# Kernel optimization log

Measured on AMD Instinct MI355X. Metric: run time of the kernel, lower is better.

## Reference

```python
import jax, jax.numpy as jnp
import numpy as np

B, N, D, K = 2, 8192, 512, 16


def setup_inputs() -> dict:
    key = jax.random.key(0)
    k1, k2, k3, k4 = jax.random.split(key, 4)
    x = jax.random.normal(k1, (B, N, D), dtype=jnp.float32)
    xyz = jax.random.normal(k2, (B, N, 3), dtype=jnp.float32)
    # nn.Linear(d_model, 3*d_model): weight [3D, D], bias [3D]
    W_qkv = jax.random.normal(k3, (3 * D, D), dtype=jnp.float32) * 0.02
    b_qkv = jnp.zeros((3 * D,), dtype=jnp.float32)
    # nn.Linear(d_model, d_model)
    W_fc = jax.random.normal(k4, (D, D), dtype=jnp.float32) * 0.02
    b_fc = jnp.zeros((D,), dtype=jnp.float32)
    return {"x": x, "xyz": xyz, "W_qkv": W_qkv, "b_qkv": b_qkv, "W_fc": W_fc, "b_fc": b_fc}


def _knn_idx(xyz):
    # squared-distance KNN (same ordering as cdist): |a|^2 + |b|^2 - 2 a.b
    sq = jnp.sum(xyz * xyz, axis=-1)                      # [B, N]
    d2 = sq[:, :, None] + sq[:, None, :] - 2.0 * jnp.einsum('bnc,bmc->bnm', xyz, xyz)
    return jax.lax.top_k(-d2, K)[1]                       # [B, N, K] smallest distances


def reference(x, xyz, W_qkv, b_qkv, W_fc, b_fc):
    knn_idx = _knn_idx(xyz)                               # no-grad in original
    qkv = jnp.einsum('bnd,ed->bne', x, W_qkv) + b_qkv     # [B, N, 3D]
    qkv = qkv.reshape(B, N, 3, D)
    q, k, v = qkv[:, :, 0], qkv[:, :, 1], qkv[:, :, 2]    # [B, N, D]
    gather = jax.vmap(lambda arr, idx: arr[idx])          # per-batch neighbor gather
    k_neigh = gather(k, knn_idx)                          # [B, N, K, D]
    v_neigh = gather(v, knn_idx)                          # [B, N, K, D]
    # faithful to einsum('bnd,bnsk->bns', q, k_neigh): sums d and feature dims independently
    attn = (q.sum(-1)[:, :, None] * k_neigh.sum(-1)) / jnp.sqrt(jnp.float32(D))  # [B, N, K]
    attn = jax.nn.softmax(attn, axis=2)[..., None]        # [B, N, K, 1]
    x_out = (attn * v_neigh).sum(axis=2)                  # [B, N, D]
    return jnp.einsum('bnd,ed->bne', x_out, W_fc) + b_fc + x
```

## Files before the change

kernel.cpp:

```cpp
#include <hip/hip_runtime.h>

typedef _Float16 half_t;
typedef _Float16 half8 __attribute__((ext_vector_type(8)));
typedef _Float16 half4v __attribute__((ext_vector_type(4)));
typedef float f32x4 __attribute__((ext_vector_type(4)));
typedef float f32x2 __attribute__((ext_vector_type(2)));

#define NB 2
#define NN 8192
#define ND 512
#define NKNN 16
#define BN (NB*NN)

#define OFF_XH   0ull
#define OFF_VH   (OFF_XH  + (size_t)BN*ND*2)
#define OFF_XOH  (OFF_VH  + (size_t)BN*ND*2)
#define OFF_WVH  (OFF_XOH + (size_t)BN*ND*2)
#define OFF_WFCH (OFF_WVH + (size_t)ND*ND*2)
#define OFF_XW   (OFF_WFCH+ (size_t)ND*ND*2)
#define OFF_XW2  (OFF_XW  + (size_t)BN*16)
#define OFF_IDX  (OFF_XW2 + (size_t)BN*16)
#define OFF_WQC  (OFF_IDX + (size_t)BN*NKNN*4)
#define OFF_WKC  (OFF_WQC + 2048)
#define OFF_QKB  (OFF_WKC + 2048)
#define OFF_QS   (OFF_QKB + 256)
#define OFF_KS   (OFF_QS  + (size_t)BN*4)

__device__ __forceinline__ void gload16(const void* g, void* l) {
  __builtin_amdgcn_global_load_lds((const __attribute__((address_space(1))) void*)g,
                                   (__attribute__((address_space(3))) void*)l, 16, 0, 0);
}

__global__ __launch_bounds__(256) void ksetup(const float* __restrict__ wqkv,
                                              const float* __restrict__ bqkv,
                                              const float* __restrict__ wfc,
                                              const float* __restrict__ xyz,
                                              float* __restrict__ wq, float* __restrict__ wk,
                                              float* __restrict__ qkb,
                                              half_t* __restrict__ wvh, half_t* __restrict__ wfch,
                                              float4* __restrict__ xw, float4* __restrict__ xw2) {
  const int blk = blockIdx.x;
  const int t = threadIdx.x;
  if (blk < 16) {
    int h = blk >> 3, g = blk & 7;
    int dl = t & 63, s = t >> 6;
    const float* Wb = wqkv + (size_t)h * 512 * 512;
    int d = g * 64 + dl;
    float acc = 0.f;
    for (int e = s * 128; e < s * 128 + 128; ++e) acc += Wb[(size_t)e * 512 + d];
    __shared__ float red[4][64];
    red[s][dl] = acc;
    __syncthreads();
    if (s == 0) (h ? wk : wq)[d] = red[0][dl] + red[1][dl] + red[2][dl] + red[3][dl];
  } else if (blk == 16) {
    __shared__ float r0[256], r1[256];
    r0[t] = bqkv[t] + bqkv[t + 256];
    r1[t] = bqkv[512 + t] + bqkv[768 + t];
    __syncthreads();
    for (int s = 128; s; s >>= 1) {
      if (t < s) { r0[t] += r0[t + s]; r1[t] += r1[t + s]; }
      __syncthreads();
    }
    if (t == 0) { qkb[0] = r0[0]; qkb[1] = r1[0]; }
  } else if (blk < 273) {
    int i = (blk - 17) * 256 + t;
    float4 a = ((const float4*)(wqkv + 1024 * 512))[i];
    half4v ha; ha[0]=(half_t)a.x; ha[1]=(half_t)a.y; ha[2]=(half_t)a.z; ha[3]=(half_t)a.w;
    *(half4v*)(wvh + (size_t)i * 4) = ha;
    float4 c = ((const float4*)wfc)[i];
    half4v hc; hc[0]=(half_t)c.x; hc[1]=(half_t)c.y; hc[2]=(half_t)c.z; hc[3]=(half_t)c.w;
    *(half4v*)(wfch + (size_t)i * 4) = hc;
  } else {
    int p = (blk - 273) * 256 + t;
    int b = p >> 12;
    int pl = p & 4095;
    int i0 = b * NN + pl * 2;
    const float* s = xyz + (size_t)i0 * 3;
    float x0 = s[0], y0 = s[1], z0 = s[2];
    float x1 = s[3], y1 = s[4], z1 = s[5];
    float sq0 = __fadd_rn(__fadd_rn(__fmul_rn(x0, x0), __fmul_rn(y0, y0)), __fmul_rn(z0, z0));
    float sq1 = __fadd_rn(__fadd_rn(__fmul_rn(x1, x1), __fmul_rn(y1, y1)), __fmul_rn(z1, z1));
    xw[i0]     = make_float4(x0, y0, z0, sq0);
    xw[i0 + 1] = make_float4(x1, y1, z1, sq1);
    xw2[(size_t)b * NN + pl]        = make_float4(x0, x1, y0, y1);
    xw2[(size_t)b * NN + NN/2 + pl] = make_float4(z0, z1, sq0, sq1);
  }
}

__global__ __launch_bounds__(256) void kxh(const float* __restrict__ x,
                                           const float* __restrict__ wq,
                                           const float* __restrict__ wk,
                                           const float* __restrict__ qkb,
                                           half_t* __restrict__ xh,
                                           float* __restrict__ qs,
                                           float* __restrict__ ks) {
  int wid = blockIdx.x * 4 + (threadIdx.x >> 6);
  int l = threadIdx.x & 63;
  size_t base = (size_t)wid * ND + l * 8;
  float4 a0 = *(const float4*)(x + base);
  float4 a1 = *(const float4*)(x + base + 4);
  half8 h;
  h[0]=(half_t)a0.x; h[1]=(half_t)a0.y; h[2]=(half_t)a0.z; h[3]=(half_t)a0.w;
  h[4]=(half_t)a1.x; h[5]=(half_t)a1.y; h[6]=(half_t)a1.z; h[7]=(half_t)a1.w;
  *(half8*)(xh + base) = h;
  float4 q0 = ((const float4*)(wq + l * 8))[0], q1 = ((const float4*)(wq + l * 8))[1];
  float4 k0 = ((const float4*)(wk + l * 8))[0], k1 = ((const float4*)(wk + l * 8))[1];
  float dq = a0.x*q0.x + a0.y*q0.y + a0.z*q0.z + a0.w*q0.w
           + a1.x*q1.x + a1.y*q1.y + a1.z*q1.z + a1.w*q1.w;
  float dk = a0.x*k0.x + a0.y*k0.y + a0.z*k0.z + a0.w*k0.w
           + a1.x*k1.x + a1.y*k1.y + a1.z*k1.z + a1.w*k1.w;
  #pragma unroll
  for (int o = 32; o; o >>= 1) { dq += __shfl_xor(dq, o); dk += __shfl_xor(dk, o); }
  if (l == 0) { qs[wid] = dq + qkb[0]; ks[wid] = dk + qkb[1]; }
}

#define QPW 4
#define KTILE 512
__global__ __launch_bounds__(256, 4) void kknn(const float4* __restrict__ xw,
                                               const float4* __restrict__ xw2,
                                               int* __restrict__ idxo) {
  __shared__ __align__(16) float4 ldsA[2][KTILE];
  __shared__ __align__(16) float4 ldsB[2][KTILE];
  __shared__ float qdl[16 * 64];
  __shared__ int   qil[16 * 64];
  const int tid = threadIdx.x;
  const int l = tid & 63;
  const int w = tid >> 6;
  const int b = blockIdx.x >> 9;
  const int qbase = (blockIdx.x & 511) * (4 * QPW) + w * QPW;
  const float4* xb  = xw  + (size_t)b * NN;
  const float4* xa2 = xw2 + (size_t)b * NN;
  const float4* xb2 = xa2 + NN / 2;

#define STAGE(t, bi) do {                                                        \
    int ts_ = (t) * KTILE;                                                       \
    gload16(xa2 + ts_ +       w * 64 + l, (void*)&ldsA[bi][      w * 64]);       \
    gload16(xa2 + ts_ + 256 + w * 64 + l, (void*)&ldsA[bi][256 + w * 64]);       \
    gload16(xb2 + ts_ +       w * 64 + l, (void*)&ldsB[bi][      w * 64]);       \
    gload16(xb2 + ts_ + 256 + w * 64 + l, (void*)&ldsB[bi][256 + w * 64]);       \
  } while (0)

  f32x2 qxx[QPW], qyy[QPW], qzz[QPW], qww[QPW];
  #pragma unroll
  for (int qi = 0; qi < QPW; ++qi) {
    float4 qp = xb[qbase + qi];
    qxx[qi] = (f32x2){qp.x, qp.x};
    qyy[qi] = (f32x2){qp.y, qp.y};
    qzz[qi] = (f32x2){qp.z, qp.z};
    qww[qi] = (f32x2){qp.w, qp.w};
  }
  const f32x2 m2 = (f32x2){-2.0f, -2.0f};

  #pragma unroll
  for (int qi = 0; qi < QPW; ++qi) {
    qdl[(w * 4 + qi) * 64 + l] = __builtin_inff();
    qil[(w * 4 + qi) * 64 + l] = 0x7fffffff;
  }

  f32x2 mind[QPW];
  #pragma unroll
  for (int qi = 0; qi < QPW; ++qi) mind[qi] = (f32x2){__builtin_inff(), __builtin_inff()};

  STAGE(0, 0);
  __syncthreads();
  for (int t = 0; t < 8; ++t) {
    if (t < 7) STAGE(t + 1, (t + 1) & 1);
    #pragma unroll
    for (int it = 0; it < 8; ++it) {
      int p = it * 64 + l;
      float4 A  = ldsA[t & 1][p];
      float4 Bv = ldsB[t & 1][p];
      f32x2 cx = (f32x2){A.x, A.y};
      f32x2 cy = (f32x2){A.z, A.w};
      f32x2 cz = (f32x2){Bv.x, Bv.y};
      f32x2 cw = (f32x2){Bv.z, Bv.w};
      #pragma unroll
      for (int qi = 0; qi < QPW; ++qi) {
        f32x2 dot = __builtin_elementwise_fma(qzz[qi], cz,
                      __builtin_elementwise_fma(qyy[qi], cy, qxx[qi] * cx));
        f32x2 s2 = qww[qi] + cw;
        f32x2 d2 = __builtin_elementwise_fma(m2, dot, s2);
        mind[qi] = __builtin_elementwise_min(mind[qi], d2);
      }
    }
    __syncthreads();
  }

  float wst[QPW];
  #pragma unroll
  for (int qi = 0; qi < QPW; ++qi) {
    float d = fminf(mind[qi][0], mind[qi][1]);
    #pragma unroll
    for (int k = 2; k <= 64; k <<= 1) {
      #pragma unroll
      for (int j = k >> 1; j > 0; j >>= 1) {
        float od = __shfl_xor(d, j);
        bool up = ((l & k) == 0);
        bool lower_lane = ((l & j) == 0);
        bool oless = od < d;
        bool take = (up == lower_lane) ? oless : !oless;
        if (take) d = od;
      }
    }
    wst[qi] = __shfl(d, 15);
  }

  int qcnt[QPW];
  #pragma unroll
  for (int qi = 0; qi < QPW; ++qi) qcnt[qi] = 0;
  const unsigned long long below = (l == 63) ? ~0ull >> 1 : (1ull << l) - 1;

  __syncthreads();
  STAGE(0, 0);
  __syncthreads();
  for (int t = 0; t < 8; ++t) {
    if (t < 7) STAGE(t + 1, (t + 1) & 1);
    #pragma unroll 2
    for (int it = 0; it < 8; ++it) {
      int p = it * 64 + l;
      float4 A  = ldsA[t & 1][p];
      float4 Bv = ldsB[t & 1][p];
      f32x2 cx = (f32x2){A.x, A.y};
      f32x2 cy = (f32x2){A.z, A.w};
      f32x2 cz = (f32x2){Bv.x, Bv.y};
      f32x2 cw = (f32x2){Bv.z, Bv.w};
      int ci0 = (t * KTILE + p) * 2;
      #pragma unroll
      for (int qi = 0; qi < QPW; ++qi) {
        f32x2 dot = __builtin_elementwise_fma(qzz[qi], cz,
                      __builtin_elementwise_fma(qyy[qi], cy, qxx[qi] * cx));
        f32x2 s2 = qww[qi] + cw;
        f32x2 d2 = __builtin_elementwise_fma(m2, dot, s2);
        bool ok0 = d2[0] <= wst[qi];
        bool ok1 = d2[1] <= wst[qi];
        unsigned long long m0 = __ballot(ok0);
        if (m0) {
          int slot = qcnt[qi] + __popcll(m0 & below);
          if (ok0 && slot < 64) {
            qdl[(w * 4 + qi) * 64 + slot] = d2[0];
            qil[(w * 4 + qi) * 64 + slot] = ci0;
          }
          qcnt[qi] += __popcll(m0);
        }
        unsigned long long m1 = __ballot(ok1);
        if (m1) {
          int slot = qcnt[qi] + __popcll(m1 & below);
          if (ok1 && slot < 64) {
            qdl[(w * 4 + qi) * 64 + slot] = d2[1];
            qil[(w * 4 + qi) * 64 + slot] = ci0 + 1;
          }
          qcnt[qi] += __popcll(m1);
        }
      }
    }
    __syncthreads();
  }

  #pragma unroll
  for (int qi = 0; qi < QPW; ++qi) {
    float d = qdl[(w * 4 + qi) * 64 + l];
    int  ii = qil[(w * 4 + qi) * 64 + l];
    #pragma unroll
    for (int k = 2; k <= 64; k <<= 1) {
      #pragma unroll
      for (int j = k >> 1; j > 0; j >>= 1) {
        float od = __shfl_xor(d, j);
        int   oi = __shfl_xor(ii, j);
        bool up = ((l & k) == 0);
        bool lower_lane = ((l & j) == 0);
        bool oless = (od < d) || (od == d && oi < ii);
        bool take = (up == lower_lane) ? oless : !oless;
        if (take) { d = od; ii = oi; }
      }
    }
    if (l < 16) idxo[((size_t)b * NN + qbase + qi) * NKNN + l] = ii;
  }
#undef STAGE
}

template <int EPI>
__global__ __launch_bounds__(256) void kgemm(const half_t* __restrict__ A,
                                             const half_t* __restrict__ Bw,
                                             const float* __restrict__ bias,
                                             const float* __restrict__ resid,
                                             void* __restrict__ Cout) {
  __shared__ __align__(16) half_t As[128 * 64];
  __shared__ __align__(16) half_t Bs[128 * 64];
  const int tid = threadIdx.x;
  const int l = tid & 63;
  const int w = tid >> 6;
  const int wm = w >> 1, wn = w & 1;
  const int mt = blockIdx.x >> 2;
  const int nt = blockIdx.x & 3;
  const int lr = l & 15, lg = l >> 4;

  f32x4 acc[4][4];
  #pragma unroll
  for (int i = 0; i < 4; ++i)
    #pragma unroll
    for (int j = 0; j < 4; ++j) acc[i][j] = (f32x4){0.f, 0.f, 0.f, 0.f};

  for (int kt = 0; kt < 8; ++kt) {
    #pragma unroll
    for (int i = 0; i < 4; ++i) {
      int id = i * 256 + tid;
      int rr = id >> 3, cc = id & 7;
      gload16(A + (size_t)(mt * 128 + rr) * ND + kt * 64 + cc * 8,
              (void*)(As + (size_t)(i * 256 + w * 64) * 8));
      gload16(Bw + (size_t)(nt * 128 + rr) * ND + kt * 64 + cc * 8,
              (void*)(Bs + (size_t)(i * 256 + w * 64) * 8));
    }
    __syncthreads();
    #pragma unroll
    for (int kk = 0; kk < 2; ++kk) {
      half8 af[4], bf[4];
      #pragma unroll
      for (int mi = 0; mi < 4; ++mi)
        af[mi] = *(const half8*)(As + (wm * 64 + mi * 16 + lr) * 64 + kk * 32 + lg * 8);
      #pragma unroll
      for (int ni = 0; ni < 4; ++ni)
        bf[ni] = *(const half8*)(Bs + (wn * 64 + ni * 16 + lr) * 64 + kk * 32 + lg * 8);
      #pragma unroll
      for (int mi = 0; mi < 4; ++mi)
        #pragma unroll
        for (int ni = 0; ni < 4; ++ni)
          acc[mi][ni] = __builtin_amdgcn_mfma_f32_16x16x32_f16(af[mi], bf[ni], acc[mi][ni], 0, 0, 0);
    }
    __syncthreads();
  }

  #pragma unroll
  for (int mi = 0; mi < 4; ++mi) {
    #pragma unroll
    for (int ni = 0; ni < 4; ++ni) {
      int col = nt * 128 + wn * 64 + ni * 16 + lr;
      #pragma unroll
      for (int r4 = 0; r4 < 4; ++r4) {
        size_t row = (size_t)mt * 128 + wm * 64 + mi * 16 + lg * 4 + r4;
        float v = acc[mi][ni][r4] + bias[col];
        if (EPI == 0) ((half_t*)Cout)[row * ND + col] = (half_t)v;
        else          ((float*)Cout)[row * ND + col] = v + resid[row * ND + col];
      }
    }
  }
}

__global__ __launch_bounds__(256) void kattn(const int* __restrict__ idx,
                                             const float* __restrict__ qs,
                                             const float* __restrict__ ks,
                                             const half_t* __restrict__ vh,
                                             half_t* __restrict__ xoh) {
  int wid = blockIdx.x * 4 + (threadIdx.x >> 6);
  int l = threadIdx.x & 63;
  int b = wid >> 13;
  int j = l & 15;
  int nb = idx[(size_t)wid * NKNN + j];
  float ksv = ks[(size_t)b * NN + nb];
  float logit = __fdiv_rn(__fmul_rn(qs[wid], ksv), 22.627416997969522f);
  float mx = logit;
  #pragma unroll
  for (int o = 8; o; o >>= 1) mx = fmaxf(mx, __shfl_xor(mx, o, 16));
  float e = expf(logit - mx);
  float s = e;
  #pragma unroll
  for (int o = 8; o; o >>= 1) s += __shfl_xor(s, o, 16);
  float p = e / s;

  float acc[8] = {0.f, 0.f, 0.f, 0.f, 0.f, 0.f, 0.f, 0.f};
  #pragma unroll
  for (int t16 = 0; t16 < 16; ++t16) {
    float wj = __shfl(p, t16, 16);
    int ij = __shfl(nb, t16, 16);
    const half8 vv = *(const half8*)(vh + ((size_t)b * NN + ij) * ND + l * 8);
    #pragma unroll
    for (int u = 0; u < 8; ++u) acc[u] += wj * (float)vv[u];
  }
  half8 ho;
  #pragma unroll
  for (int u = 0; u < 8; ++u) ho[u] = (half_t)acc[u];
  *(half8*)(xoh + (size_t)wid * ND + l * 8) = ho;
}

extern "C" void kernel_launch(void* const* d_in, const int* in_sizes, int n_in,
                              void* d_out, int out_size, void* d_ws, size_t ws_size,
                              hipStream_t stream) {
  const float* x    = (const float*)d_in[0];
  const float* xyz  = (const float*)d_in[1];
  const float* wqkv = (const float*)d_in[2];
  const float* bqkv = (const float*)d_in[3];
  const float* wfc  = (const float*)d_in[4];
  const float* bfc  = (const float*)d_in[5];
  char* ws = (char*)d_ws;
  half_t* xh   = (half_t*)(ws + OFF_XH);
  half_t* vh   = (half_t*)(ws + OFF_VH);
  half_t* xoh  = (half_t*)(ws + OFF_XOH);
  half_t* wvh  = (half_t*)(ws + OFF_WVH);
  half_t* wfch = (half_t*)(ws + OFF_WFCH);
  float4* xw   = (float4*)(ws + OFF_XW);
  float4* xw2  = (float4*)(ws + OFF_XW2);
  int*    idx  = (int*)(ws + OFF_IDX);
  float*  wqc  = (float*)(ws + OFF_WQC);
  float*  wkc  = (float*)(ws + OFF_WKC);
  float*  qkb  = (float*)(ws + OFF_QKB);
  float*  qs   = (float*)(ws + OFF_QS);
  float*  ks   = (float*)(ws + OFF_KS);

  ksetup<<<dim3(305), dim3(256), 0, stream>>>(wqkv, bqkv, wfc, xyz,
                                              wqc, wkc, qkb, wvh, wfch, xw, xw2);
  kxh   <<<dim3(4096),dim3(256), 0, stream>>>(x, wqc, wkc, qkb, xh, qs, ks);
  kknn  <<<dim3(1024),dim3(256), 0, stream>>>(xw, xw2, idx);
  kgemm<0><<<dim3(512),dim3(256), 0, stream>>>(xh, wvh, bqkv + 1024, (const float*)nullptr, (void*)vh);
  kattn <<<dim3(4096),dim3(256), 0, stream>>>(idx, qs, ks, vh, xoh);
  kgemm<1><<<dim3(512),dim3(256), 0, stream>>>(xoh, wfch, bfc, x, d_out);
}
```

Baseline: 145.3 us.

## Fold output projection into value projection to drop the final GEMM

Result: no change. 142.9 us (median of 2 runs) (-1.7%).

```diff
diff --git a/kernel.cpp b/kernel.cpp
--- a/kernel.cpp
+++ b/kernel.cpp
@@ -25,6 +25,8 @@
 #define OFF_QKB  (OFF_WKC + 2048)
 #define OFF_QS   (OFF_QKB + 256)
 #define OFF_KS   (OFF_QS  + (size_t)BN*4)
+#define OFF_WCB  OFF_XOH
+#define OFF_BCB  (OFF_XOH + (size_t)ND*ND*2)
 
 __device__ __forceinline__ void gload16(const void* g, void* l) {
   __builtin_amdgcn_global_load_lds((const __attribute__((address_space(1))) void*)g,
@@ -37,8 +39,9 @@
                                               const float* __restrict__ xyz,
                                               float* __restrict__ wq, float* __restrict__ wk,
                                               float* __restrict__ qkb,
-                                              half_t* __restrict__ wvh, half_t* __restrict__ wfch,
-                                              float4* __restrict__ xw, float4* __restrict__ xw2) {
+                                              half_t* __restrict__ wvth, half_t* __restrict__ wfch,
+                                              float4* __restrict__ xw, float4* __restrict__ xw2,
+                                              float* __restrict__ bcomb) {
   const int blk = blockIdx.x;
   const int t = threadIdx.x;
   if (blk < 16) {
@@ -64,13 +67,10 @@
     if (t == 0) { qkb[0] = r0[0]; qkb[1] = r1[0]; }
   } else if (blk < 273) {
     int i = (blk - 17) * 256 + t;
-    float4 a = ((const float4*)(wqkv + 1024 * 512))[i];
-    half4v ha; ha[0]=(half_t)a.x; ha[1]=(half_t)a.y; ha[2]=(half_t)a.z; ha[3]=(half_t)a.w;
-    *(half4v*)(wvh + (size_t)i * 4) = ha;
     float4 c = ((const float4*)wfc)[i];
     half4v hc; hc[0]=(half_t)c.x; hc[1]=(half_t)c.y; hc[2]=(half_t)c.z; hc[3]=(half_t)c.w;
     *(half4v*)(wfch + (size_t)i * 4) = hc;
-  } else {
+  } else if (blk < 305) {
     int p = (blk - 273) * 256 + t;
     int b = p >> 12;
     int pl = p & 4095;
@@ -84,6 +84,31 @@
     xw[i0 + 1] = make_float4(x1, y1, z1, sq1);
     xw2[(size_t)b * NN + pl]        = make_float4(x0, x1, y0, y1);
     xw2[(size_t)b * NN + NN/2 + pl] = make_float4(z0, z1, sq0, sq1);
+  } else if (blk < 369) {
+    int tile = blk - 305, tr = tile >> 3, tc = tile & 7;
+    __shared__ float tbuf[64][65];
+    int rr = t >> 6, cc = t & 63;
+    #pragma unroll 4
+    for (int p = 0; p < 16; ++p)
+      tbuf[p * 4 + rr][cc] = wqkv[(size_t)(1024 + tc * 64 + p * 4 + rr) * 512 + tr * 64 + cc];
+    __syncthreads();
+    #pragma unroll 4
+    for (int p = 0; p < 16; ++p)
+      wvth[(size_t)(tr * 64 + p * 4 + rr) * 512 + tc * 64 + cc] = (half_t)tbuf[cc][p * 4 + rr];
+  } else {
+    int base = (blk - 369) * 8;
+    int wv_ = t >> 6, l_ = t & 63;
+    #pragma unroll
+    for (int rr = 0; rr < 2; ++rr) {
+      int e = base + wv_ * 2 + rr;
+      float acc = 0.f;
+      #pragma unroll
+      for (int it = 0; it < 8; ++it)
+        acc += wfc[(size_t)e * 512 + it * 64 + l_] * bqkv[1024 + it * 64 + l_];
+      #pragma unroll
+      for (int o = 32; o; o >>= 1) acc += __shfl_xor(acc, o);
+      if (l_ == 0) bcomb[e] = acc;
+    }
   }
 }
 
@@ -208,7 +233,7 @@
   int qcnt[QPW];
   #pragma unroll
   for (int qi = 0; qi < QPW; ++qi) qcnt[qi] = 0;
-  const unsigned long long below = (l == 63) ? ~0ull >> 1 : (1ull << l) - 1;
+  const unsigned long long below = (1ull << l) - 1;
 
   __syncthreads();
   STAGE(0, 0);
@@ -282,7 +307,6 @@
 __global__ __launch_bounds__(256) void kgemm(const half_t* __restrict__ A,
                                              const half_t* __restrict__ Bw,
                                              const float* __restrict__ bias,
-                                             const float* __restrict__ resid,
                                              void* __restrict__ Cout) {
   __shared__ __align__(16) half_t As[128 * 64];
   __shared__ __align__(16) half_t Bs[128 * 64];
@@ -337,9 +361,8 @@
       #pragma unroll
       for (int r4 = 0; r4 < 4; ++r4) {
         size_t row = (size_t)mt * 128 + wm * 64 + mi * 16 + lg * 4 + r4;
-        float v = acc[mi][ni][r4] + bias[col];
-        if (EPI == 0) ((half_t*)Cout)[row * ND + col] = (half_t)v;
-        else          ((float*)Cout)[row * ND + col] = v + resid[row * ND + col];
+        if (EPI == 0) ((half_t*)Cout)[row * ND + col] = (half_t)(acc[mi][ni][r4] + bias[col]);
+        else          ((half_t*)Cout)[row * ND + col] = (half_t)acc[mi][ni][r4];
       }
     }
   }
@@ -348,8 +371,10 @@
 __global__ __launch_bounds__(256) void kattn(const int* __restrict__ idx,
                                              const float* __restrict__ qs,
                                              const float* __restrict__ ks,
-                                             const half_t* __restrict__ vh,
-                                             half_t* __restrict__ xoh) {
+                                             const half_t* __restrict__ vfh,
+                                             const float* __restrict__ bfc,
+                                             const float* __restrict__ x,
+                                             float* __restrict__ out) {
   int wid = blockIdx.x * 4 + (threadIdx.x >> 6);
   int l = threadIdx.x & 63;
   int b = wid >> 13;
@@ -371,14 +396,21 @@
   for (int t16 = 0; t16 < 16; ++t16) {
     float wj = __shfl(p, t16, 16);
     int ij = __shfl(nb, t16, 16);
-    const half8 vv = *(const half8*)(vh + ((size_t)b * NN + ij) * ND + l * 8);
+    const half8 vv = *(const half8*)(vfh + ((size_t)b * NN + ij) * ND + l * 8);
     #pragma unroll
     for (int u = 0; u < 8; ++u) acc[u] += wj * (float)vv[u];
   }
-  half8 ho;
-  #pragma unroll
-  for (int u = 0; u < 8; ++u) ho[u] = (half_t)acc[u];
-  *(half8*)(xoh + (size_t)wid * ND + l * 8) = ho;
+  size_t base = (size_t)wid * ND + l * 8;
+  float4 xa0 = *(const float4*)(x + base);
+  float4 xa1 = *(const float4*)(x + base + 4);
+  float4 bf0 = *(const float4*)(bfc + l * 8);
+  float4 bf1 = *(const float4*)(bfc + l * 8 + 4);
+  float4 o0 = make_float4(acc[0] + bf0.x + xa0.x, acc[1] + bf0.y + xa0.y,
+                          acc[2] + bf0.z + xa0.z, acc[3] + bf0.w + xa0.w);
+  float4 o1 = make_float4(acc[4] + bf1.x + xa1.x, acc[5] + bf1.y + xa1.y,
+                          acc[6] + bf1.z + xa1.z, acc[7] + bf1.w + xa1.w);
+  *(float4*)(out + base) = o0;
+  *(float4*)(out + base + 4) = o1;
 }
 
 extern "C" void kernel_launch(void* const* d_in, const int* in_sizes, int n_in,
@@ -391,25 +423,26 @@
   const float* wfc  = (const float*)d_in[4];
   const float* bfc  = (const float*)d_in[5];
   char* ws = (char*)d_ws;
-  half_t* xh   = (half_t*)(ws + OFF_XH);
-  half_t* vh   = (half_t*)(ws + OFF_VH);
-  half_t* xoh  = (half_t*)(ws + OFF_XOH);
-  half_t* wvh  = (half_t*)(ws + OFF_WVH);
-  half_t* wfch = (half_t*)(ws + OFF_WFCH);
-  float4* xw   = (float4*)(ws + OFF_XW);
-  float4* xw2  = (float4*)(ws + OFF_XW2);
-  int*    idx  = (int*)(ws + OFF_IDX);
-  float*  wqc  = (float*)(ws + OFF_WQC);
-  float*  wkc  = (float*)(ws + OFF_WKC);
-  float*  qkb  = (float*)(ws + OFF_QKB);
-  float*  qs   = (float*)(ws + OFF_QS);
-  float*  ks   = (float*)(ws + OFF_KS);
-
-  ksetup<<<dim3(305), dim3(256), 0, stream>>>(wqkv, bqkv, wfc, xyz,
-                                              wqc, wkc, qkb, wvh, wfch, xw, xw2);
-  kxh   <<<dim3(4096),dim3(256), 0, stream>>>(x, wqc, wkc, qkb, xh, qs, ks);
-  kknn  <<<dim3(1024),dim3(256), 0, stream>>>(xw, xw2, idx);
-  kgemm<0><<<dim3(512),dim3(256), 0, stream>>>(xh, wvh, bqkv + 1024, (const float*)nullptr, (void*)vh);
-  kattn <<<dim3(4096),dim3(256), 0, stream>>>(idx, qs, ks, vh, xoh);
-  kgemm<1><<<dim3(512),dim3(256), 0, stream>>>(xoh, wfch, bfc, x, d_out);
-}
+  half_t* xh    = (half_t*)(ws + OFF_XH);
+  half_t* vfh   = (half_t*)(ws + OFF_VH);
+  half_t* wvth  = (half_t*)(ws + OFF_WVH);
+  half_t* wfch  = (half_t*)(ws + OFF_WFCH);
+  half_t* wcomb = (half_t*)(ws + OFF_WCB);
+  float*  bcomb = (float*)(ws + OFF_BCB);
+  float4* xw    = (float4*)(ws + OFF_XW);
+  float4* xw2   = (float4*)(ws + OFF_XW2);
+  int*    idx   = (int*)(ws + OFF_IDX);
+  float*  wqc   = (float*)(ws + OFF_WQC);
+  float*  wkc   = (float*)(ws + OFF_WKC);
+  float*  qkb   = (float*)(ws + OFF_QKB);
+  float*  qs    = (float*)(ws + OFF_QS);
+  float*  ks    = (float*)(ws + OFF_KS);
+
+  ksetup<<<dim3(433), dim3(256), 0, stream>>>(wqkv, bqkv, wfc, xyz,
+                                              wqc, wkc, qkb, wvth, wfch, xw, xw2, bcomb);
+  kxh     <<<dim3(4096),dim3(256), 0, stream>>>(x, wqc, wkc, qkb, xh, qs, ks);
+  kknn    <<<dim3(1024),dim3(256), 0, stream>>>(xw, xw2, idx);
+  kgemm<2><<<dim3(16),  dim3(256), 0, stream>>>(wfch, wvth, (const float*)nullptr, (void*)wcomb);
+  kgemm<0><<<dim3(512), dim3(256), 0, stream>>>(xh, wcomb, bcomb, (void*)vfh);
+  kattn   <<<dim3(4096),dim3(256), 0, stream>>>(idx, qs, ks, vfh, bfc, x, (float*)d_out);
+}
```
